# Kernel optimization log

Hardware: AMD Instinct MI355X
Metric: run time of the kernel (lower is better)

## Reference

```python
import jax, jax.numpy as jnp
import numpy as np

B, T, FD, NH, NC, NOUT = 32, 512, 256, 1024, 512, 8


def setup_inputs() -> dict:
    key = jax.random.key(0)
    ks = jax.random.split(key, 12)
    s = lambda k, sh, sc=0.05: (jax.random.normal(k, sh, jnp.float32) * sc)
    return dict(
        x=jax.random.normal(ks[0], (B, T, FD), jnp.float32),
        lens=jax.random.randint(ks[1], (B,), T // 2, T + 1, jnp.int32),
        W1=s(ks[2], (NH, FD)), b1=jnp.zeros((NH,), jnp.float32),
        g1=jnp.ones((NH,), jnp.float32), be1=jnp.zeros((NH,), jnp.float32),
        W2=s(ks[3], (NH, NH)), b2=jnp.zeros((NH,), jnp.float32),
        g2=jnp.ones((NH,), jnp.float32), be2=jnp.zeros((NH,), jnp.float32),
        lstm_wih=s(ks[4], (2, 2, 4 * NC, NH)),   # [layer, dir, 4H, in]
        lstm_whh=s(ks[5], (2, 2, 4 * NC, NC)),   # [layer, dir, 4H, H]
        lstm_bih=s(ks[6], (2, 2, 4 * NC)),
        lstm_bhh=s(ks[7], (2, 2, 4 * NC)),
        w_u=s(ks[8], (2 * NC,)), b_u=jnp.zeros((), jnp.float32),
        Wc=s(ks[9], (NOUT, 2 * NC)), bc=jnp.zeros((NOUT,), jnp.float32),
    )


def _layernorm(x, g, b, eps=1e-5):
    m = x.mean(-1, keepdims=True)
    v = ((x - m) ** 2).mean(-1, keepdims=True)
    return (x - m) / jnp.sqrt(v + eps) * g + b


def _lrelu(z):
    return jnp.where(z >= 0, z, 0.01 * z)  # LeakyReLU default slope


def _lstm_dir(x, wih, whh, bih, bhh):
    # x: [B,T,in] -> h: [B,T,H]; torch gate order i,f,g,o
    Bz = x.shape[0]
    H = whh.shape[1]
    xp = jnp.einsum('bti,gi->btg', x, wih) + bih + bhh  # [B,T,4H]

    def step(carry, xt):
        h, c = carry
        gates = xt + h @ whh.T
        i, f, g, o = jnp.split(gates, 4, axis=-1)
        c = jax.nn.sigmoid(f) * c + jax.nn.sigmoid(i) * jnp.tanh(g)
        h = jax.nn.sigmoid(o) * jnp.tanh(c)
        return (h, c), h

    h0 = jnp.zeros((Bz, H), x.dtype)
    _, hs = jax.lax.scan(step, (h0, h0), xp.transpose(1, 0, 2))
    return hs.transpose(1, 0, 2)


def _bilstm(x, wih, whh, bih, bhh):
    # params indexed [dir, ...]; backward dir processes the full padded
    # sequence reversed (original feeds unpacked pad_sequence to nn.LSTM)
    hf = _lstm_dir(x, wih[0], whh[0], bih[0], bhh[0])
    hb = _lstm_dir(x[:, ::-1], wih[1], whh[1], bih[1], bhh[1])[:, ::-1]
    return jnp.concatenate([hf, hb], axis=-1)


def reference(x, lens, W1, b1, g1, be1, W2, b2, g2, be2,
              lstm_wih, lstm_whh, lstm_bih, lstm_bhh, w_u, b_u, Wc, bc):
    Tn = x.shape[1]
    # extract MLP (dropout = identity in eval)
    h = _lrelu(_layernorm(x @ W1.T + b1, g1, be1))
    h = _lrelu(_layernorm(h @ W2.T + b2, g2, be2))
    # pad_sequence zero-pads AFTER extract -> zero out pad positions
    mask = jnp.arange(Tn)[None, :] < lens[:, None]  # [B,T]
    h = h * mask[..., None]
    # 2-layer bidirectional LSTM over the full padded sequence
    h = _bilstm(h, lstm_wih[0], lstm_whh[0], lstm_bih[0], lstm_bhh[0])
    h = _bilstm(h, lstm_wih[1], lstm_whh[1], lstm_bih[1], lstm_bhh[1])
    # Attn with window_len=1: per-step linear score, masked softmax, weighted sum
    scores = h @ w_u + b_u                          # [B,T]
    scores = jnp.where(mask, scores, -jnp.inf)
    alpha = jax.nn.softmax(scores, axis=-1)
    pooled = jnp.einsum('bt,btd->bd', alpha, h)     # [B, 2*NC]
    return pooled @ Wc.T + bc
```

## Files before the change

### kernel.cpp

```cpp
#include <hip/hip_runtime.h>
#include <stdint.h>
#include <stddef.h>


typedef short  short8  __attribute__((ext_vector_type(8)));
typedef short  short4v __attribute__((ext_vector_type(4)));
typedef float  float4v __attribute__((ext_vector_type(4)));
typedef unsigned long long u64;

__device__ inline float b2f(short x){
  union { unsigned u; float f; } v; v.u = ((unsigned)(unsigned short)x) << 16; return v.f;
}
__device__ inline short f2b(float f){
  union { float f; unsigned u; } v; v.f = f;
  unsigned r = (v.u + 0x7fffu + ((v.u >> 16) & 1u)) >> 16;
  return (short)r;
}
__device__ inline float sigm(float x){ return 1.f / (1.f + __expf(-x)); }
__device__ inline float tanh_(float x){ return 2.f / (1.f + __expf(-2.f*x)) - 1.f; }

__global__ __launch_bounds__(256) void detect_f32(
    const unsigned short* __restrict__ p, unsigned* __restrict__ flag)
{
  const int tid = threadIdx.x;
  unsigned h = 0;
  for (int i = tid; i < 1024; i += 256){
    const unsigned e = (p[i] >> 7) & 0xFFu;
    if (e >= 0xC0u) ++h;
  }
#pragma unroll
  for (int off=32; off>0; off>>=1) h += __shfl_xor(h, off, 64);
  __shared__ unsigned sh[4];
  if ((tid&63)==0) sh[tid>>6] = h;
  __syncthreads();
  if (tid==0) *flag = (sh[0]+sh[1]+sh[2]+sh[3] >= 8u) ? 1u : 0u;
}

__global__ __launch_bounds__(256) void to_bf16(
    const void* __restrict__ src, short* __restrict__ dst, int n,
    const unsigned* __restrict__ flag)
{
  const int i = blockIdx.x*256 + threadIdx.x;
  if (i >= n) return;
  if (*flag) dst[i] = f2b(((const float*)src)[i]);
  else       dst[i] = ((const short*)src)[i];
}

__global__ __launch_bounds__(256) void gemm_bt(
    const short* __restrict__ A, const short* __restrict__ W,
    short* __restrict__ C, const short* __restrict__ bias1,
    const short* __restrict__ bias2, int N, int K)
{
  __shared__ __align__(16) short lA[128*40];
  __shared__ __align__(16) short lW[128*40];
  const int tid  = threadIdx.x;
  const int lane = tid & 63, wv = tid >> 6;
  const int wm = wv >> 1, wn = wv & 1;
  const int quad = lane >> 4, l15 = lane & 15;
  const long m0 = (long)blockIdx.y * 128, n0 = (long)blockIdx.x * 128;

  float4v acc[4][4];
#pragma unroll
  for (int i=0;i<4;++i)
#pragma unroll
    for (int j=0;j<4;++j) acc[i][j] = (float4v)0.f;

  const int r  = tid >> 2;
  const int kc = tid & 3;
  const int nkt = K >> 5;
  for (int kt = 0; kt < nkt; ++kt) {
    __syncthreads();
    const short* ga = A + (m0 + r) * (long)K + kt*32 + kc*8;
    const short* gw = W + (n0 + r) * (long)K + kt*32 + kc*8;
    short8 a0 = *(const short8*)ga;
    short8 a1 = *(const short8*)(ga + 64*(long)K);
    short8 w0 = *(const short8*)gw;
    short8 w1 = *(const short8*)(gw + 64*(long)K);
    *(short8*)&lA[r*40 + kc*8]        = a0;
    *(short8*)&lA[(r+64)*40 + kc*8]   = a1;
    *(short8*)&lW[r*40 + kc*8]        = w0;
    *(short8*)&lW[(r+64)*40 + kc*8]   = w1;
    __syncthreads();
    short8 af[4], bfr[4];
#pragma unroll
    for (int i=0;i<4;++i) af[i]  = *(const short8*)&lA[(wm*64 + i*16 + l15)*40 + quad*8];
#pragma unroll
    for (int j=0;j<4;++j) bfr[j] = *(const short8*)&lW[(wn*64 + j*16 + l15)*40 + quad*8];
#pragma unroll
    for (int i=0;i<4;++i)
#pragma unroll
      for (int j=0;j<4;++j)
        acc[i][j] = __builtin_amdgcn_mfma_f32_16x16x32_bf16(af[i], bfr[j], acc[i][j], 0, 0, 0);
  }
#pragma unroll
  for (int j=0;j<4;++j){
    const long n = n0 + wn*64 + j*16 + l15;
    float bs = b2f(bias1[n]);
    if (bias2) bs += b2f(bias2[n]);
#pragma unroll
    for (int i=0;i<4;++i){
      const long mb = m0 + wm*64 + i*16 + quad*4;
#pragma unroll
      for (int g=0; g<4; ++g)
        C[(mb+g)*(long)N + n] = f2b(acc[i][j][g] + bs);
    }
  }
}

__global__ __launch_bounds__(256) void ln_lrelu(
    const short* __restrict__ X, const short* __restrict__ g,
    const short* __restrict__ be, short* __restrict__ out,
    const int* __restrict__ lens, const int domask)
{
  const int row = blockIdx.x, tid = threadIdx.x;
  const short* xr = X + (size_t)row * 1024;
  short4v xv = *(const short4v*)(xr + tid*4);
  float v[4];
#pragma unroll
  for (int k=0;k<4;++k) v[k] = b2f(xv[k]);
  float s  = v[0]+v[1]+v[2]+v[3];
  float sq = v[0]*v[0]+v[1]*v[1]+v[2]*v[2]+v[3]*v[3];
#pragma unroll
  for (int off=32; off>0; off>>=1){
    s  += __shfl_xor(s,  off, 64);
    sq += __shfl_xor(sq, off, 64);
  }
  __shared__ float red[8];
  if ((tid&63)==0){ red[tid>>6] = s; red[4+(tid>>6)] = sq; }
  __syncthreads();
  s  = red[0]+red[1]+red[2]+red[3];
  sq = red[4]+red[5]+red[6]+red[7];
  const float mean = s * (1.f/1024.f);
  const float var  = sq * (1.f/1024.f) - mean*mean;
  const float rstd = rsqrtf(var + 1e-5f);
  float zmul = 1.f;
  if (domask){ const int b = row >> 9, t = row & 511; if (t >= lens[b]) zmul = 0.f; }
  short4v o;
#pragma unroll
  for (int k=0;k<4;++k){
    const int n = tid*4 + k;
    float y = (v[k]-mean)*rstd*b2f(g[n]) + b2f(be[n]);
    y = (y >= 0.f) ? y : 0.01f*y;
    o[k] = f2b(y * zmul);
  }
  *(short4v*)(out + (size_t)row*1024 + tid*4) = o;
}

__global__ __launch_bounds__(256) void lstm_scan(
    const short* __restrict__ xp, const int xp_cols, const int dir0,
    const short* __restrict__ whh,
    u64* __restrict__ hstate,
    short* __restrict__ hout,
    const unsigned epoch)
{
  const int wg = blockIdx.x;
  const int dloc = wg >> 5, d = dir0 + dloc;
  const int u0 = (wg & 31) * 16;
  const int tid = threadIdx.x, lane = tid & 63, wv = tid >> 6;
  const int quad = lane >> 4, l15 = lane & 15;

  short8 af[16];
  {
    const short* wr = whh + ((size_t)d*2048 + wv*512 + u0 + l15)*512 + quad*8;
#pragma unroll
    for (int ks=0; ks<16; ++ks) af[ks] = *(const short8*)(wr + ks*32);
  }

  const int bb = tid >> 3, pp = tid & 7;
  float cstA = 0.f, cstB = 0.f;
  __shared__ __align__(16) unsigned hsh[2][32*260];
  __shared__ float gl[4][16][33];
  const unsigned tbase = epoch << 10;

  for (int step=0; step<512; ++step){
    const int t = d ? (511-step) : step;
    short4v x0, x1;
    {
      const size_t gb = (size_t)dloc*2048 + (size_t)wv*512 + u0 + quad*4;
      x0 = *(const short4v*)(xp + ((size_t)l15*512      + t)*xp_cols + gb);
      x1 = *(const short4v*)(xp + ((size_t)(l15+16)*512 + t)*xp_cols + gb);
    }
    unsigned* stg = &hsh[step&1][tid];
    if (step == 0){
#pragma unroll
      for (int k=0;k<32;++k) stg[k*260] = 0u;
    } else {
      const u64* hq = hstate + ((size_t)(d*2 + (step&1))<<13) + tid;
      const unsigned tgt = tbase + (unsigned)step;
      u64 v[32];
      for(;;){
        unsigned ok = 1u;
#pragma unroll
        for (int k=0;k<32;++k)
          v[k] = __hip_atomic_load(hq + (size_t)k*256,
                                   __ATOMIC_RELAXED, __HIP_MEMORY_SCOPE_AGENT);
#pragma unroll
        for (int k=0;k<32;++k) ok &= (unsigned)((unsigned)(v[k] >> 32) == tgt);
        if (ok) break;
        __builtin_amdgcn_s_sleep(1);
      }
#pragma unroll
      for (int k=0;k<32;++k) stg[k*260] = (unsigned)v[k];
    }
    __syncthreads();

    float4v acc0, acc1;
#pragma unroll
    for (int g=0; g<4; ++g){ acc0[g] = b2f(x0[g]); acc1[g] = b2f(x1[g]); }
    const short* hs = (const short*)&hsh[step&1][0];
#pragma unroll
    for (int ks=0; ks<16; ++ks){
      short8 b0 = *(const short8*)(hs + (size_t)l15*520      + ks*32 + quad*8);
      short8 b1 = *(const short8*)(hs + (size_t)(l15+16)*520 + ks*32 + quad*8);
      acc0 = __builtin_amdgcn_mfma_f32_16x16x32_bf16(af[ks], b0, acc0, 0, 0, 0);
      acc1 = __builtin_amdgcn_mfma_f32_16x16x32_bf16(af[ks], b1, acc1, 0, 0, 0);
    }
#pragma unroll
    for (int g=0; g<4; ++g){
      gl[wv][quad*4+g][l15]    = acc0[g];
      gl[wv][quad*4+g][l15+16] = acc1[g];
    }
    __syncthreads();

    float hv[2];
#pragma unroll
    for (int i=0; i<2; ++i){
      const int uu = 2*pp + i;
      const float gi = gl[0][uu][bb], gf = gl[1][uu][bb];
      const float gg = gl[2][uu][bb], go = gl[3][uu][bb];
      float& cref = i ? cstB : cstA;
      const float c = sigm(gf)*cref + sigm(gi)*tanh_(gg);
      cref = c;
      hv[i] = sigm(go) * tanh_(c);
    }
    const unsigned hw = (unsigned)(unsigned short)f2b(hv[0])
                      | ((unsigned)(unsigned short)f2b(hv[1]) << 16);
    const u64 pkt = ((u64)(tbase + (unsigned)step + 1u) << 32) | (u64)hw;
    __hip_atomic_store(hstate + ((size_t)(d*2 + ((step+1)&1))<<13)
                         + (size_t)bb*256 + (u0>>1) + pp,
                       pkt, __ATOMIC_RELAXED, __HIP_MEMORY_SCOPE_AGENT);
    *(unsigned*)&hout[((size_t)bb*512 + t)*1024 + d*512 + u0 + 2*pp] = hw;
  }
}

__global__ __launch_bounds__(256) void attn_cls(
    const short* __restrict__ hseq, const short* __restrict__ wu,
    const short* __restrict__ Wc, const short* __restrict__ bc,
    const int* __restrict__ lens, float* __restrict__ out)
{
  const int b = blockIdx.x, tid = threadIdx.x, lane = tid & 63, wv = tid >> 6;
  const int len = lens[b];
  __shared__ float wus[1024];
  __shared__ float sc[512];
  __shared__ float redx[8];
  __shared__ float pooled[1024];
  for (int i=tid; i<1024; i+=256) wus[i] = b2f(wu[i]);
  __syncthreads();
  const short* hb = hseq + (size_t)b*512*1024;
  for (int t=wv; t<512; t+=4){
    const short* hr = hb + (size_t)t*1024;
    float s = 0.f;
#pragma unroll
    for (int j=0;j<16;++j) s += b2f(hr[lane + j*64]) * wus[lane + j*64];
#pragma unroll
    for (int off=32; off>0; off>>=1) s += __shfl_xor(s, off, 64);
    if (lane==0) sc[t] = (t < len) ? s : -3.0e38f;
  }
  __syncthreads();
  float m = -3.0e38f;
  for (int i=tid;i<512;i+=256) m = fmaxf(m, sc[i]);
#pragma unroll
  for (int off=32; off>0; off>>=1) m = fmaxf(m, __shfl_xor(m, off, 64));
  if (lane==0) redx[wv] = m;
  __syncthreads();
  m = fmaxf(fmaxf(redx[0],redx[1]), fmaxf(redx[2],redx[3]));
  float ssum = 0.f;
  for (int i=tid;i<512;i+=256){
    float e = (i<len) ? __expf(sc[i]-m) : 0.f;
    sc[i] = e;
    ssum += e;
  }
#pragma unroll
  for (int off=32; off>0; off>>=1) ssum += __shfl_xor(ssum, off, 64);
  if (lane==0) redx[4+wv] = ssum;
  __syncthreads();
  ssum = redx[4]+redx[5]+redx[6]+redx[7];
  const float inv = 1.f/ssum;
  float4v pa = (float4v)0.f;
  const int k0 = tid*4;
  for (int t=0; t<len; ++t){
    const float a = sc[t];
    short4v hv = *(const short4v*)(hb + (size_t)t*1024 + k0);
    pa[0] += a*b2f(hv[0]); pa[1] += a*b2f(hv[1]);
    pa[2] += a*b2f(hv[2]); pa[3] += a*b2f(hv[3]);
  }
  pooled[k0+0] = pa[0]*inv; pooled[k0+1] = pa[1]*inv;
  pooled[k0+2] = pa[2]*inv; pooled[k0+3] = pa[3]*inv;
  __syncthreads();
  const int j = tid >> 5, l32 = tid & 31;
  float s2 = 0.f;
  for (int kk=l32; kk<1024; kk+=32) s2 += b2f(Wc[j*1024+kk]) * pooled[kk];
#pragma unroll
  for (int off=16; off>0; off>>=1) s2 += __shfl_xor(s2, off, 32);
  if (l32==0) out[b*8+j] = s2 + b2f(bc[j]);
}

extern "C" void kernel_launch(void* const* d_in, const int* in_sizes, int n_in,
                              void* d_out, int out_size, void* d_ws, size_t ws_size,
                              hipStream_t stream)
{
  (void)in_sizes; (void)n_in; (void)out_size;
  const int*   lens = (const int*)d_in[1];
  float* outp = (float*)d_out;

  const size_t SZ_XP_A = (size_t)16384*4096*2;
  const size_t SZ_XP_B = (size_t)16384*2048*2;
  const size_t SZ_H    = (size_t)16384*1024*2;
  const size_t SZ_HS   = 262144;
  const size_t SZ_CNT  = 16384;
  const size_t SZ_NORM = 37000000;
  const bool planA = ws_size >= SZ_XP_A + 2*SZ_H + SZ_HS + SZ_CNT + SZ_NORM;
  const bool planB = !planA && ws_size >= SZ_XP_B + 2*SZ_H + SZ_HS + SZ_CNT + SZ_NORM;
  if (!planA && !planB) return;
  const size_t xpsz = planA ? SZ_XP_A : SZ_XP_B;

  char* ws = (char*)d_ws;
  short*    XP  = (short*)ws;
  short*    HB  = (short*)(ws + xpsz);
  short*    HC  = (short*)(ws + xpsz + SZ_H);
  u64*      HS64= (u64*)(ws + xpsz + 2*SZ_H);
  unsigned* CNT = (unsigned*)(ws + xpsz + 2*SZ_H + SZ_HS);
  unsigned* FLAG = CNT + 4000;
  short*    pool = (short*)(ws + xpsz + 2*SZ_H + SZ_HS + SZ_CNT);

  size_t off = 0;
  auto carve = [&](size_t n){ short* p = pool + off; off += (n + 127) & ~(size_t)127; return p; };
  short* x   = carve(4194304);
  short* W1  = carve(262144);
  short* b1  = carve(1024);
  short* g1  = carve(1024);
  short* be1 = carve(1024);
  short* W2  = carve(1048576);
  short* b2  = carve(1024);
  short* g2  = carve(1024);
  short* be2 = carve(1024);
  short* wih = carve(8388608);
  short* whh = carve(4194304);
  short* bih = carve(8192);
  short* bhh = carve(8192);
  short* wu  = carve(1024);
  short* Wc  = carve(8192);
  short* bc  = carve(8);

  hipMemsetAsync(HS64, 0, SZ_HS, stream);
  detect_f32<<<1, 256, 0, stream>>>((const unsigned short*)d_in[0], FLAG);

  struct { int idx; short* dst; int n; } cv[16] = {
    {0,x,4194304},{2,W1,262144},{3,b1,1024},{4,g1,1024},{5,be1,1024},
    {6,W2,1048576},{7,b2,1024},{8,g2,1024},{9,be2,1024},
    {10,wih,8388608},{11,whh,4194304},{12,bih,8192},{13,bhh,8192},
    {14,wu,1024},{16,Wc,8192},{17,bc,8}
  };
  for (int i=0;i<16;++i)
    to_bf16<<<(cv[i].n + 255)/256, 256, 0, stream>>>(d_in[cv[i].idx], cv[i].dst, cv[i].n, FLAG);

  dim3 blk(256);
  gemm_bt<<<dim3(8,128),  blk, 0, stream>>>(x,  W1, XP, b1, nullptr, 1024, 256);
  ln_lrelu<<<16384, blk, 0, stream>>>(XP, g1, be1, HB, lens, 0);
  gemm_bt<<<dim3(8,128),  blk, 0, stream>>>(HB, W2, XP, b2, nullptr, 1024, 1024);
  ln_lrelu<<<16384, blk, 0, stream>>>(XP, g2, be2, HC, lens, 1);

  const short* lin[2]  = { HC, HB };
  short*       lout[2] = { HB, HC };
  for (int l = 0; l < 2; ++l){
    const short* whh_l = whh + (size_t)l*2*2048*512;
    if (planA){
      gemm_bt<<<dim3(32,128), blk, 0, stream>>>(
          lin[l], wih + (size_t)l*4096*1024, XP,
          bih + l*4096, bhh + l*4096, 4096, 1024);
      lstm_scan<<<64, blk, 0, stream>>>(XP, 4096, 0, whh_l, HS64, lout[l],
                                        (unsigned)(l+1));
    } else {
      for (int d = 0; d < 2; ++d){
        gemm_bt<<<dim3(16,128), blk, 0, stream>>>(
            lin[l], wih + ((size_t)(l*2+d))*2048*1024, XP,
            bih + (l*2+d)*2048, bhh + (l*2+d)*2048, 2048, 1024);
        lstm_scan<<<32, blk, 0, stream>>>(XP, 2048, d, whh_l, HS64, lout[l],
                                          (unsigned)(l+1));
      }
    }
  }
  attn_cls<<<32, blk, 0, stream>>>(HC, wu, Wc, bc, lens, outp);
}
```

Before: 4.215 ms.

## Interleave LSTM gate rows per unit to keep gate math in registers

Permutes the LSTM weight and bias rows so the four gates of each hidden unit sit next to each other. Each MFMA output lane then holds i,f,g,o for one unit and batch, so the cell update runs directly in registers. This removes the shared-memory gate exchange and the second __syncthreads per recurrent step. It also splits the K-loop into two independent accumulator chains for more MFMA overlap, and changes the hidden-state exchange layout so each thread polls 32 contiguous words. The cost is an extra permuting conversion pass over the weights and a shuffle to pack the bf16 pairs.

```diff
diff --git a/kernel.cpp b/kernel.cpp
--- a/kernel.cpp
+++ b/kernel.cpp
@@ -44,6 +44,21 @@
   if (i >= n) return;
   if (*flag) dst[i] = f2b(((const float*)src)[i]);
   else       dst[i] = ((const short*)src)[i];
+}
+
+__global__ __launch_bounds__(256) void to_bf16_perm(
+    const void* __restrict__ src, short* __restrict__ dst, const int W,
+    const int n, const unsigned* __restrict__ flag)
+{
+  const int i = blockIdx.x*256 + threadIdx.x;
+  if (i >= n) return;
+  const int col = i % W;
+  const int r   = (i / W) % 2048;
+  const int blk = i / (W * 2048);
+  const int gate = r >> 9, unit = r & 511;
+  const size_t j = ((size_t)blk*2048 + (size_t)(unit*4 + gate))*W + col;
+  short out = (*flag) ? f2b(((const float*)src)[i]) : ((const short*)src)[i];
+  dst[j] = out;
 }
 
 __global__ __launch_bounds__(256) void gemm_bt(
@@ -161,22 +176,24 @@
 
   short8 af[16];
   {
-    const short* wr = whh + ((size_t)d*2048 + wv*512 + u0 + l15)*512 + quad*8;
+    const int unit = u0 + wv*4 + (l15 >> 2);
+    const int prow = unit*4 + (l15 & 3);
+    const short* wr = whh + ((size_t)d*2048 + prow)*512 + quad*8;
 #pragma unroll
     for (int ks=0; ks<16; ++ks) af[ks] = *(const short8*)(wr + ks*32);
   }
 
-  const int bb = tid >> 3, pp = tid & 7;
   float cstA = 0.f, cstB = 0.f;
   __shared__ __align__(16) unsigned hsh[2][32*260];
-  __shared__ float gl[4][16][33];
   const unsigned tbase = epoch << 10;
+  const int pair = (u0 >> 1) + wv*2 + (quad >> 1);
+  const int bst  = l15 + ((quad & 1) << 4);
 
   for (int step=0; step<512; ++step){
     const int t = d ? (511-step) : step;
     short4v x0, x1;
     {
-      const size_t gb = (size_t)dloc*2048 + (size_t)wv*512 + u0 + quad*4;
+      const size_t gb = (size_t)dloc*2048 + (size_t)(u0 + wv*4 + quad)*4;
       x0 = *(const short4v*)(xp + ((size_t)l15*512      + t)*xp_cols + gb);
       x1 = *(const short4v*)(xp + ((size_t)(l15+16)*512 + t)*xp_cols + gb);
     }
@@ -185,14 +202,14 @@
 #pragma unroll
       for (int k=0;k<32;++k) stg[k*260] = 0u;
     } else {
-      const u64* hq = hstate + ((size_t)(d*2 + (step&1))<<13) + tid;
+      const u64* hq = hstate + ((size_t)(d*2 + (step&1))<<13) + (size_t)tid*32;
       const unsigned tgt = tbase + (unsigned)step;
       u64 v[32];
       for(;;){
         unsigned ok = 1u;
 #pragma unroll
         for (int k=0;k<32;++k)
-          v[k] = __hip_atomic_load(hq + (size_t)k*256,
+          v[k] = __hip_atomic_load(hq + k,
                                    __ATOMIC_RELAXED, __HIP_MEMORY_SCOPE_AGENT);
 #pragma unroll
         for (int k=0;k<32;++k) ok &= (unsigned)((unsigned)(v[k] >> 32) == tgt);
@@ -204,42 +221,45 @@
     }
     __syncthreads();
 
-    float4v acc0, acc1;
-#pragma unroll
-    for (int g=0; g<4; ++g){ acc0[g] = b2f(x0[g]); acc1[g] = b2f(x1[g]); }
+    float4v a0e, a0o, a1e, a1o;
+#pragma unroll
+    for (int g=0; g<4; ++g){
+      a0e[g] = b2f(x0[g]); a1e[g] = b2f(x1[g]);
+      a0o[g] = 0.f;        a1o[g] = 0.f;
+    }
     const short* hs = (const short*)&hsh[step&1][0];
 #pragma unroll
-    for (int ks=0; ks<16; ++ks){
-      short8 b0 = *(const short8*)(hs + (size_t)l15*520      + ks*32 + quad*8);
-      short8 b1 = *(const short8*)(hs + (size_t)(l15+16)*520 + ks*32 + quad*8);
-      acc0 = __builtin_amdgcn_mfma_f32_16x16x32_bf16(af[ks], b0, acc0, 0, 0, 0);
-      acc1 = __builtin_amdgcn_mfma_f32_16x16x32_bf16(af[ks], b1, acc1, 0, 0, 0);
-    }
-#pragma unroll
-    for (int g=0; g<4; ++g){
-      gl[wv][quad*4+g][l15]    = acc0[g];
-      gl[wv][quad*4+g][l15+16] = acc1[g];
-    }
-    __syncthreads();
-
-    float hv[2];
-#pragma unroll
-    for (int i=0; i<2; ++i){
-      const int uu = 2*pp + i;
-      const float gi = gl[0][uu][bb], gf = gl[1][uu][bb];
-      const float gg = gl[2][uu][bb], go = gl[3][uu][bb];
-      float& cref = i ? cstB : cstA;
-      const float c = sigm(gf)*cref + sigm(gi)*tanh_(gg);
-      cref = c;
-      hv[i] = sigm(go) * tanh_(c);
-    }
-    const unsigned hw = (unsigned)(unsigned short)f2b(hv[0])
-                      | ((unsigned)(unsigned short)f2b(hv[1]) << 16);
-    const u64 pkt = ((u64)(tbase + (unsigned)step + 1u) << 32) | (u64)hw;
+    for (int kp=0; kp<8; ++kp){
+      short8 b0e = *(const short8*)(hs + (size_t)l15*520      + (2*kp)*32   + quad*8);
+      short8 b0o = *(const short8*)(hs + (size_t)l15*520      + (2*kp+1)*32 + quad*8);
+      short8 b1e = *(const short8*)(hs + (size_t)(l15+16)*520 + (2*kp)*32   + quad*8);
+      short8 b1o = *(const short8*)(hs + (size_t)(l15+16)*520 + (2*kp+1)*32 + quad*8);
+      a0e = __builtin_amdgcn_mfma_f32_16x16x32_bf16(af[2*kp],   b0e, a0e, 0, 0, 0);
+      a0o = __builtin_amdgcn_mfma_f32_16x16x32_bf16(af[2*kp+1], b0o, a0o, 0, 0, 0);
+      a1e = __builtin_amdgcn_mfma_f32_16x16x32_bf16(af[2*kp],   b1e, a1e, 0, 0, 0);
+      a1o = __builtin_amdgcn_mfma_f32_16x16x32_bf16(af[2*kp+1], b1o, a1o, 0, 0, 0);
+    }
+
+    const float gi0 = a0e[0]+a0o[0], gf0 = a0e[1]+a0o[1];
+    const float gg0 = a0e[2]+a0o[2], go0 = a0e[3]+a0o[3];
+    const float gi1 = a1e[0]+a1o[0], gf1 = a1e[1]+a1o[1];
+    const float gg1 = a1e[2]+a1o[2], go1 = a1e[3]+a1o[3];
+    cstA = sigm(gf0)*cstA + sigm(gi0)*tanh_(gg0);
+    const float h0 = sigm(go0)*tanh_(cstA);
+    cstB = sigm(gf1)*cstB + sigm(gi1)*tanh_(gg1);
+    const float h1 = sigm(go1)*tanh_(cstB);
+
+    const unsigned own = (unsigned)(unsigned short)f2b(h0)
+                       | ((unsigned)(unsigned short)f2b(h1) << 16);
+    const unsigned oth = __shfl_xor(own, 16, 64);
+    const unsigned payload = (quad & 1)
+        ? ((oth >> 16) | (own & 0xFFFF0000u))
+        : ((own & 0xFFFFu) | (oth << 16));
+    const u64 pkt = ((u64)(tbase + (unsigned)step + 1u) << 32) | (u64)payload;
     __hip_atomic_store(hstate + ((size_t)(d*2 + ((step+1)&1))<<13)
-                         + (size_t)bb*256 + (u0>>1) + pp,
+                         + (size_t)pair*32 + bst,
                        pkt, __ATOMIC_RELAXED, __HIP_MEMORY_SCOPE_AGENT);
-    *(unsigned*)&hout[((size_t)bb*512 + t)*1024 + d*512 + u0 + 2*pp] = hw;
+    *(unsigned*)&hout[((size_t)bst*512 + t)*1024 + d*512 + 2*pair] = payload;
   }
 }
 
@@ -355,14 +375,19 @@
   hipMemsetAsync(HS64, 0, SZ_HS, stream);
   detect_f32<<<1, 256, 0, stream>>>((const unsigned short*)d_in[0], FLAG);
 
-  struct { int idx; short* dst; int n; } cv[16] = {
+  struct { int idx; short* dst; int n; } cv[12] = {
     {0,x,4194304},{2,W1,262144},{3,b1,1024},{4,g1,1024},{5,be1,1024},
     {6,W2,1048576},{7,b2,1024},{8,g2,1024},{9,be2,1024},
-    {10,wih,8388608},{11,whh,4194304},{12,bih,8192},{13,bhh,8192},
     {14,wu,1024},{16,Wc,8192},{17,bc,8}
   };
-  for (int i=0;i<16;++i)
+  for (int i=0;i<12;++i)
     to_bf16<<<(cv[i].n + 255)/256, 256, 0, stream>>>(d_in[cv[i].idx], cv[i].dst, cv[i].n, FLAG);
+  struct { int idx; short* dst; int W; int n; } pv[4] = {
+    {10,wih,1024,8388608},{11,whh,512,4194304},{12,bih,1,8192},{13,bhh,1,8192}
+  };
+  for (int i=0;i<4;++i)
+    to_bf16_perm<<<(pv[i].n + 255)/256, 256, 0, stream>>>(d_in[pv[i].idx], pv[i].dst,
+                                                          pv[i].W, pv[i].n, FLAG);
 
   dim3 blk(256);
   gemm_bt<<<dim3(8,128),  blk, 0, stream>>>(x,  W1, XP, b1, nullptr, 1024, 256);
```

New measurement: 7.602 ms. 80.4% more time.
